# Kernel optimization log

Measured on AMD Instinct MI355X. Metric: run time of the kernel, lower is better.

The kernel has to match this reference:

```python
import jax, jax.numpy as jnp
import numpy as np

N = 1 << 20          # rays (1024x1024 image)
H = 128              # SDF MLP hidden dim
NEAR, FAR = 0.2, 2.0
ALPHA = 100.0
ITERS = 32           # sphere_march iters
EPS = 0.005
TP_BATCH = 32        # throughput batch_size
RAND_U = 0.5         # fixed replacement for random.random() in throughput


def setup_inputs() -> dict:
    key = jax.random.key(0)
    ks = jax.random.split(key, 6)
    def w(k, shape):
        return jax.random.normal(k, shape, jnp.float32) * (1.0 / np.sqrt(shape[0]))
    return {
        "rays": jax.random.normal(ks[0], (N, 6), jnp.float32),
        # SDF MLP: 3 -> H -> H -> 1 (output squeezed to scalar per point)
        "W1": w(ks[1], (3, H)), "b1": jnp.zeros((H,), jnp.float32),
        "W2": w(ks[2], (H, H)), "b2": jnp.zeros((H,), jnp.float32),
        "W3": w(ks[3], (H, 1)), "b3": jnp.zeros((1,), jnp.float32),
        # reflectance MLP: concat(pts, dir)=6 -> H -> 3
        "R1": w(ks[4], (6, H)), "rb1": jnp.zeros((H,), jnp.float32),
        "R2": w(ks[5], (H, 3)), "rb2": jnp.zeros((3,), jnp.float32),
    }


def _sdf(x, W1, b1, W2, b2, W3, b3):
    h = jax.nn.relu(x @ W1 + b1)
    h = jax.nn.relu(h @ W2 + b2)
    return (h @ W3 + b3)[..., 0]          # [N]


def _refl(x, d, R1, rb1, R2, rb2):
    h = jax.nn.relu(jnp.concatenate([x, d], axis=-1) @ R1 + rb1)
    return h @ R2 + rb2                    # [N, 3]


def reference(rays, W1, b1, W2, b2, W3, b3, R1, rb1, R2, rb2):
    r_o, r_d = rays[..., :3], rays[..., 3:]
    sg = jax.lax.stop_gradient
    # marching loops run under torch.no_grad -> use stop_gradient'd operands
    ro_s, rd_s = sg(r_o), sg(r_d)
    sdf_ng = lambda p: _sdf(p, sg(W1), sg(b1), sg(W2), sg(b2), sg(W3), sg(b3))

    # ---- sphere_march ----
    def march_body(i, carry):
        hits, cd = carry                                  # [N,1] bool, [N,1] f32
        dist = sdf_ng(ro_s + rd_s * cd)[..., None]
        hits = hits | ((dist < EPS) & (cd >= NEAR) & (cd <= FAR))
        cd = jnp.where(hits, cd, cd + dist)
        return hits, cd

    hits0 = jnp.zeros((rays.shape[0], 1), bool)
    cd0 = jnp.full((rays.shape[0], 1), NEAR, jnp.float32)
    hits, cd = jax.lax.fori_loop(0, ITERS, march_body, (hits0, cd0))

    pts = r_o + r_d * cd                                  # grads flow via r_o, r_d
    rgb = _refl(pts, r_d, R1, rb1, R2, rb2)               # [N,3]
    out = jnp.where(hits, rgb, jnp.zeros_like(rgb))

    # ---- throughput ----
    max_t = FAR + RAND_U * (2.0 / TP_BATCH)
    step = max_t / TP_BATCH

    def tp_body(i, carry):
        curr_min, idxs = carry                            # [N] f32, [N] i32
        sd = sdf_ng(ro_s + (step * (i + 1)) * rd_s)
        idxs = jnp.where(sd < curr_min, i + 1, idxs)
        curr_min = jnp.minimum(curr_min, sd)
        return curr_min, idxs

    sd0 = sdf_ng(ro_s)
    _, idxs = jax.lax.fori_loop(0, TP_BATCH, tp_body,
                                (sd0, jnp.zeros(sd0.shape, jnp.int32)))
    best_pos = r_o + idxs[..., None].astype(jnp.float32) * step * r_d
    tput = _sdf(best_pos, W1, b1, W2, b2, W3, b3)         # [N]

    return jnp.concatenate([out, -ALPHA * tput[..., None]], axis=-1)  # [N,4]
```

## Files before the change

### kernel.cpp

```cpp
#include <hip/hip_runtime.h>

typedef __attribute__((ext_vector_type(8))) short bf16x8;
typedef __attribute__((ext_vector_type(4))) float f32x4;
typedef __attribute__((ext_vector_type(2))) float f32x2;

constexpr int   HD      = 128;
constexpr float T_NEAR  = 0.2f;
constexpr float T_FAR   = 2.0f;
constexpr float ALPHA_C = 100.0f;
constexpr int   MARCH_N = 32;
constexpr float HIT_EPS = 0.005f;
constexpr int   TP_N    = 32;
constexpr float STEP    = 0.0634765625f;

__device__ __forceinline__ unsigned short f2bf(float x) {
  unsigned u = __float_as_uint(x);
  unsigned r = 0x7fffu + ((u >> 16) & 1u);
  return (unsigned short)((u + r) >> 16);
}

union U8 { bf16x8 v; uint4 u4; unsigned short us[8]; };

__device__ __forceinline__ f32x2 pk_fma(f32x2 a, f32x2 b, f32x2 c) {
  f32x2 d;
  asm("v_pk_fma_f32 %0, %1, %2, %3" : "=v"(d) : "v"(a), "v"(b), "v"(c));
  return d;
}

__device__ __forceinline__ unsigned pack_relu_pair(f32x2 h) {
  unsigned u0 = __float_as_uint(h.x) + 0x8000u;
  unsigned u1 = __float_as_uint(h.y) + 0x8000u;
  unsigned w, r;
  asm("v_perm_b32 %0, %1, %2, %3" : "=v"(w) : "v"(u1), "v"(u0), "s"(0x07060302u));
  asm("v_pk_max_i16 %0, %1, %2" : "=v"(r) : "v"(w), "v"(0u));
  return r;
}

__global__ void pack_w2(const float* __restrict__ W2,
                        unsigned short* __restrict__ hi,
                        unsigned short* __restrict__ lo) {
  int idx = blockIdx.x * 256 + threadIdx.x;
  int j = idx & 7, l = (idx >> 3) & 63, t = (idx >> 9) & 7, s = idx >> 12;
  int m = 16 * t + (l & 15);
  int k = 32 * s + (l >> 4) * 8 + j;
  float w = W2[k * HD + m];
  unsigned short h = f2bf(w);
  float hf = __uint_as_float(((unsigned)h) << 16);
  hi[idx] = h;
  lo[idx] = f2bf(w - hf);
}

__device__ __forceinline__ float sdf_fast(float t,
    const bf16x8 (&w2f)[4][8], const f32x2 (&ap)[16], const f32x2 (&cp)[16],
    const f32x4 (&b2f)[8], const f32x2 (&w3p)[16], float b3v)
{
  f32x2 t2; t2.x = t; t2.y = t;
  U8 B[4];
  #pragma unroll
  for (int s = 0; s < 4; ++s) {
    unsigned w0 = pack_relu_pair(pk_fma(cp[4*s+0], t2, ap[4*s+0]));
    unsigned w1 = pack_relu_pair(pk_fma(cp[4*s+1], t2, ap[4*s+1]));
    unsigned w2 = pack_relu_pair(pk_fma(cp[4*s+2], t2, ap[4*s+2]));
    unsigned w3 = pack_relu_pair(pk_fma(cp[4*s+3], t2, ap[4*s+3]));
    uint4 u; u.x = w0; u.y = w1; u.z = w2; u.w = w3;
    B[s].u4 = u;
  }

  f32x4 acc[8];
  #pragma unroll
  for (int u = 0; u < 8; ++u)
    acc[u] = __builtin_amdgcn_mfma_f32_16x16x32_bf16(w2f[0][u], B[0].v, b2f[u], 0, 0, 0);
  #pragma unroll
  for (int s = 1; s < 4; ++s)
    #pragma unroll
    for (int u = 0; u < 8; ++u)
      acc[u] = __builtin_amdgcn_mfma_f32_16x16x32_bf16(w2f[s][u], B[s].v, acc[u], 0, 0, 0);

  f32x2 e0; e0.x = 0.f; e0.y = 0.f;
  f32x2 e1 = e0, e2 = e0, e3 = e0;
  #pragma unroll
  for (int u = 0; u < 8; ++u) {
    f32x4 y = acc[u];
    f32x2 lo; lo.x = fmaxf(y.x, 0.f); lo.y = fmaxf(y.y, 0.f);
    f32x2 hi; hi.x = fmaxf(y.z, 0.f); hi.y = fmaxf(y.w, 0.f);
    if (u & 1) { e2 = pk_fma(lo, w3p[2*u], e2); e3 = pk_fma(hi, w3p[2*u+1], e3); }
    else       { e0 = pk_fma(lo, w3p[2*u], e0); e1 = pk_fma(hi, w3p[2*u+1], e1); }
  }
  float d = (e0.x + e0.y) + (e1.x + e1.y) + ((e2.x + e2.y) + (e3.x + e3.y));
  d += __shfl_xor(d, 16);
  d += __shfl_xor(d, 32);
  return d + b3v;
}

__device__ float sdf_precise(float t, int lane,
    const bf16x8 (&w2f)[4][8], const f32x2 (&ap)[16], const f32x2 (&cp)[16],
    const f32x4 (&b2f)[8], const f32x2 (&w3p)[16], float b3v,
    const unsigned short* __restrict__ wlo)
{
  U8 HH[4], HL[4];
  #pragma unroll
  for (int s = 0; s < 4; ++s) {
    #pragma unroll
    for (int p = 0; p < 4; ++p) {
      float h0 = fmaxf(fmaf(cp[4*s+p].x, t, ap[4*s+p].x), 0.f);
      float h1 = fmaxf(fmaf(cp[4*s+p].y, t, ap[4*s+p].y), 0.f);
      unsigned short hb0 = f2bf(h0), hb1 = f2bf(h1);
      float r0 = h0 - __uint_as_float(((unsigned)hb0) << 16);
      float r1 = h1 - __uint_as_float(((unsigned)hb1) << 16);
      HH[s].us[2*p]     = hb0;      HH[s].us[2*p + 1] = hb1;
      HL[s].us[2*p]     = f2bf(r0); HL[s].us[2*p + 1] = f2bf(r1);
    }
  }

  const bf16x8* wloF = (const bf16x8*)wlo;
  f32x4 acc[8];
  #pragma unroll
  for (int u = 0; u < 8; ++u)
    acc[u] = __builtin_amdgcn_mfma_f32_16x16x32_bf16(w2f[0][u], HH[0].v, b2f[u], 0, 0, 0);
  #pragma unroll
  for (int s = 0; s < 4; ++s) {
    #pragma unroll
    for (int u = 0; u < 8; ++u) {
      bf16x8 wl = wloF[(s * 8 + u) * 64 + lane];
      if (s > 0)
        acc[u] = __builtin_amdgcn_mfma_f32_16x16x32_bf16(w2f[s][u], HH[s].v, acc[u], 0, 0, 0);
      acc[u] = __builtin_amdgcn_mfma_f32_16x16x32_bf16(wl, HH[s].v, acc[u], 0, 0, 0);
      acc[u] = __builtin_amdgcn_mfma_f32_16x16x32_bf16(w2f[s][u], HL[s].v, acc[u], 0, 0, 0);
    }
  }

  f32x2 e0; e0.x = 0.f; e0.y = 0.f;
  f32x2 e1 = e0, e2 = e0, e3 = e0;
  #pragma unroll
  for (int u = 0; u < 8; ++u) {
    f32x4 y = acc[u];
    f32x2 lo; lo.x = fmaxf(y.x, 0.f); lo.y = fmaxf(y.y, 0.f);
    f32x2 hi; hi.x = fmaxf(y.z, 0.f); hi.y = fmaxf(y.w, 0.f);
    if (u & 1) { e2 = pk_fma(lo, w3p[2*u], e2); e3 = pk_fma(hi, w3p[2*u+1], e3); }
    else       { e0 = pk_fma(lo, w3p[2*u], e0); e1 = pk_fma(hi, w3p[2*u+1], e1); }
  }
  float d = (e0.x + e0.y) + (e1.x + e1.y) + ((e2.x + e2.y) + (e3.x + e3.y));
  d += __shfl_xor(d, 16);
  d += __shfl_xor(d, 32);
  return d + b3v;
}

__global__ __launch_bounds__(256, 1)
void render(const float* __restrict__ rays,
            const float* __restrict__ W1, const float* __restrict__ b1,
            const float* __restrict__ b2, const float* __restrict__ W3,
            const float* __restrict__ b3,
            const float* __restrict__ R1, const float* __restrict__ rb1,
            const float* __restrict__ R2, const float* __restrict__ rb2,
            const unsigned short* __restrict__ whi,
            const unsigned short* __restrict__ wlo,
            float* __restrict__ out, int nrays)
{
  const int tid  = threadIdx.x;
  const int lane = tid & 63;
  const int q    = lane >> 4;
  const int wv   = tid >> 6;
  const int ray  = blockIdx.x * 64 + wv * 16 + (lane & 15);

  bf16x8 w2f[4][8];
  const bf16x8* whiF = (const bf16x8*)whi;
  #pragma unroll
  for (int s = 0; s < 4; ++s)
    #pragma unroll
    for (int u = 0; u < 8; ++u)
      w2f[s][u] = whiF[(s * 8 + u) * 64 + lane];

  const float rox = rays[ray * 6 + 0];
  const float roy = rays[ray * 6 + 1];
  const float roz = rays[ray * 6 + 2];
  const float rdx = rays[ray * 6 + 3];
  const float rdy = rays[ray * 6 + 4];
  const float rdz = rays[ray * 6 + 5];
  const float b3v = b3[0];

  f32x2 ap[16], cp[16];
  #pragma unroll
  for (int s = 0; s < 4; ++s)
    #pragma unroll
    for (int p = 0; p < 4; ++p) {
      int k0 = 32 * s + 8 * q + 2 * p;
      int k1 = k0 + 1;
      float x0 = W1[k0], y0 = W1[HD + k0], z0 = W1[2 * HD + k0];
      float x1 = W1[k1], y1 = W1[HD + k1], z1 = W1[2 * HD + k1];
      f32x2 a, c;
      a.x = fmaf(x0, rox, fmaf(y0, roy, fmaf(z0, roz, b1[k0])));
      a.y = fmaf(x1, rox, fmaf(y1, roy, fmaf(z1, roz, b1[k1])));
      c.x = fmaf(x0, rdx, fmaf(y0, rdy, z0 * rdz));
      c.y = fmaf(x1, rdx, fmaf(y1, rdy, z1 * rdz));
      ap[4 * s + p] = a;
      cp[4 * s + p] = c;
    }

  f32x4 b2f[8];
  f32x2 w3p[16];
  #pragma unroll
  for (int u = 0; u < 8; ++u) {
    int n0 = 16 * u + 4 * q;
    f32x4 bb; bb.x = b2[n0]; bb.y = b2[n0 + 1]; bb.z = b2[n0 + 2]; bb.w = b2[n0 + 3];
    b2f[u] = bb;
    f32x2 wa; wa.x = W3[n0];     wa.y = W3[n0 + 1];
    f32x2 wb; wb.x = W3[n0 + 2]; wb.y = W3[n0 + 3];
    w3p[2 * u] = wa; w3p[2 * u + 1] = wb;
  }

  float cd = T_NEAR;
  bool hit = false;
  #pragma unroll 1
  for (int it = 0; it < MARCH_N; ++it) {
    float d = sdf_fast(cd, w2f, ap, cp, b2f, w3p, b3v);
    bool nh = (d < HIT_EPS) && (cd >= T_NEAR) && (cd <= T_FAR);
    hit = hit || nh;
    cd = hit ? cd : cd + d;
    if (__ballot(!hit) == 0ull) break;
  }

  const float ptx = fmaf(rdx, cd, rox);
  const float pty = fmaf(rdy, cd, roy);
  const float ptz = fmaf(rdz, cd, roz);
  float cr = 0.f, cg = 0.f, cb = 0.f;
  {
    int jb = q * 32;
    #pragma unroll 1
    for (int jj = 0; jj < 32; ++jj) {
      int j = jb + jj;
      float h = fmaf(R1[0 * HD + j], ptx,
                fmaf(R1[1 * HD + j], pty,
                fmaf(R1[2 * HD + j], ptz,
                fmaf(R1[3 * HD + j], rdx,
                fmaf(R1[4 * HD + j], rdy,
                fmaf(R1[5 * HD + j], rdz, rb1[j]))))));
      h = fmaxf(h, 0.f);
      cr = fmaf(h, R2[j * 3 + 0], cr);
      cg = fmaf(h, R2[j * 3 + 1], cg);
      cb = fmaf(h, R2[j * 3 + 2], cb);
    }
    cr += __shfl_xor(cr, 16); cr += __shfl_xor(cr, 32);
    cg += __shfl_xor(cg, 16); cg += __shfl_xor(cg, 32);
    cb += __shfl_xor(cb, 16); cb += __shfl_xor(cb, 32);
    cr += rb2[0]; cg += rb2[1]; cb += rb2[2];
  }

  float mn = sdf_fast(0.f, w2f, ap, cp, b2f, w3p, b3v);
  int idx = 0;
  float ts = 0.f;
  #pragma unroll 1
  for (int s = 1; s <= TP_N; ++s) {
    ts += STEP;
    float d = sdf_fast(ts, w2f, ap, cp, b2f, w3p, b3v);
    if (d < mn) { mn = d; idx = s; }
  }

  const float tb = STEP * (float)idx;
  const float tput = sdf_precise(tb, lane, w2f, ap, cp, b2f, w3p, b3v, wlo);

  if (q == 0) {
    float4 o;
    o.x = hit ? cr : 0.f;
    o.y = hit ? cg : 0.f;
    o.z = hit ? cb : 0.f;
    o.w = -ALPHA_C * tput;
    ((float4*)out)[ray] = o;
  }
}

extern "C" void kernel_launch(void* const* d_in, const int* in_sizes, int n_in,
                              void* d_out, int out_size, void* d_ws, size_t ws_size,
                              hipStream_t stream) {
  const float* rays = (const float*)d_in[0];
  const float* W1  = (const float*)d_in[1];
  const float* b1  = (const float*)d_in[2];
  const float* W2  = (const float*)d_in[3];
  const float* b2  = (const float*)d_in[4];
  const float* W3  = (const float*)d_in[5];
  const float* b3  = (const float*)d_in[6];
  const float* R1  = (const float*)d_in[7];
  const float* rb1 = (const float*)d_in[8];
  const float* R2  = (const float*)d_in[9];
  const float* rb2 = (const float*)d_in[10];

  unsigned short* whi = (unsigned short*)d_ws;
  unsigned short* wlo = whi + 128 * 128;

  const int nrays = in_sizes[0] / 6;

  hipLaunchKernelGGL(pack_w2, dim3(64), dim3(256), 0, stream, W2, whi, wlo);
  hipLaunchKernelGGL(render, dim3(nrays / 64), dim3(256), 0, stream,
                     rays, W1, b1, b2, W3, b3, R1, rb1, R2, rb2,
                     whi, wlo, (float*)d_out, nrays);
}
```

Before: 3.413 ms.

## Process two ray groups per wave with interleaved MFMA chains

```diff
diff --git a/kernel.cpp b/kernel.cpp
--- a/kernel.cpp
+++ b/kernel.cpp
@@ -50,32 +50,8 @@
   lo[idx] = f2bf(w - hf);
 }
 
-__device__ __forceinline__ float sdf_fast(float t,
-    const bf16x8 (&w2f)[4][8], const f32x2 (&ap)[16], const f32x2 (&cp)[16],
-    const f32x4 (&b2f)[8], const f32x2 (&w3p)[16], float b3v)
-{
-  f32x2 t2; t2.x = t; t2.y = t;
-  U8 B[4];
-  #pragma unroll
-  for (int s = 0; s < 4; ++s) {
-    unsigned w0 = pack_relu_pair(pk_fma(cp[4*s+0], t2, ap[4*s+0]));
-    unsigned w1 = pack_relu_pair(pk_fma(cp[4*s+1], t2, ap[4*s+1]));
-    unsigned w2 = pack_relu_pair(pk_fma(cp[4*s+2], t2, ap[4*s+2]));
-    unsigned w3 = pack_relu_pair(pk_fma(cp[4*s+3], t2, ap[4*s+3]));
-    uint4 u; u.x = w0; u.y = w1; u.z = w2; u.w = w3;
-    B[s].u4 = u;
-  }
-
-  f32x4 acc[8];
-  #pragma unroll
-  for (int u = 0; u < 8; ++u)
-    acc[u] = __builtin_amdgcn_mfma_f32_16x16x32_bf16(w2f[0][u], B[0].v, b2f[u], 0, 0, 0);
-  #pragma unroll
-  for (int s = 1; s < 4; ++s)
-    #pragma unroll
-    for (int u = 0; u < 8; ++u)
-      acc[u] = __builtin_amdgcn_mfma_f32_16x16x32_bf16(w2f[s][u], B[s].v, acc[u], 0, 0, 0);
-
+__device__ __forceinline__ float sdf_reduce(const f32x4 (&acc)[8],
+                                            const f32x2 (&w3p)[16], float b3v) {
   f32x2 e0; e0.x = 0.f; e0.y = 0.f;
   f32x2 e1 = e0, e2 = e0, e3 = e0;
   #pragma unroll
@@ -92,7 +68,51 @@
   return d + b3v;
 }
 
-__device__ float sdf_precise(float t, int lane,
+__device__ __forceinline__ void sdf_fast_dual(float tA, float tB,
+    const bf16x8 (&w2f)[4][8],
+    const f32x2 (&apA)[16], const f32x2 (&cpA)[16],
+    const f32x2 (&apB)[16], const f32x2 (&cpB)[16],
+    const f32x4 (&b2f)[8], const f32x2 (&w3p)[16], float b3v,
+    float& dA, float& dB)
+{
+  f32x2 tA2; tA2.x = tA; tA2.y = tA;
+  f32x2 tB2; tB2.x = tB; tB2.y = tB;
+  U8 BA[4], BB[4];
+  #pragma unroll
+  for (int s = 0; s < 4; ++s) {
+    uint4 ua;
+    ua.x = pack_relu_pair(pk_fma(cpA[4*s+0], tA2, apA[4*s+0]));
+    ua.y = pack_relu_pair(pk_fma(cpA[4*s+1], tA2, apA[4*s+1]));
+    ua.z = pack_relu_pair(pk_fma(cpA[4*s+2], tA2, apA[4*s+2]));
+    ua.w = pack_relu_pair(pk_fma(cpA[4*s+3], tA2, apA[4*s+3]));
+    BA[s].u4 = ua;
+    uint4 ub;
+    ub.x = pack_relu_pair(pk_fma(cpB[4*s+0], tB2, apB[4*s+0]));
+    ub.y = pack_relu_pair(pk_fma(cpB[4*s+1], tB2, apB[4*s+1]));
+    ub.z = pack_relu_pair(pk_fma(cpB[4*s+2], tB2, apB[4*s+2]));
+    ub.w = pack_relu_pair(pk_fma(cpB[4*s+3], tB2, apB[4*s+3]));
+    BB[s].u4 = ub;
+  }
+
+  f32x4 accA[8], accB[8];
+  #pragma unroll
+  for (int u = 0; u < 8; ++u) {
+    accA[u] = __builtin_amdgcn_mfma_f32_16x16x32_bf16(w2f[0][u], BA[0].v, b2f[u], 0, 0, 0);
+    accB[u] = __builtin_amdgcn_mfma_f32_16x16x32_bf16(w2f[0][u], BB[0].v, b2f[u], 0, 0, 0);
+  }
+  #pragma unroll
+  for (int s = 1; s < 4; ++s)
+    #pragma unroll
+    for (int u = 0; u < 8; ++u) {
+      accA[u] = __builtin_amdgcn_mfma_f32_16x16x32_bf16(w2f[s][u], BA[s].v, accA[u], 0, 0, 0);
+      accB[u] = __builtin_amdgcn_mfma_f32_16x16x32_bf16(w2f[s][u], BB[s].v, accB[u], 0, 0, 0);
+    }
+
+  dA = sdf_reduce(accA, w3p, b3v);
+  dB = sdf_reduce(accB, w3p, b3v);
+}
+
+__device__ __forceinline__ float sdf_precise(float t, int lane,
     const bf16x8 (&w2f)[4][8], const f32x2 (&ap)[16], const f32x2 (&cp)[16],
     const f32x4 (&b2f)[8], const f32x2 (&w3p)[16], float b3v,
     const unsigned short* __restrict__ wlo)
@@ -129,20 +149,7 @@
     }
   }
 
-  f32x2 e0; e0.x = 0.f; e0.y = 0.f;
-  f32x2 e1 = e0, e2 = e0, e3 = e0;
-  #pragma unroll
-  for (int u = 0; u < 8; ++u) {
-    f32x4 y = acc[u];
-    f32x2 lo; lo.x = fmaxf(y.x, 0.f); lo.y = fmaxf(y.y, 0.f);
-    f32x2 hi; hi.x = fmaxf(y.z, 0.f); hi.y = fmaxf(y.w, 0.f);
-    if (u & 1) { e2 = pk_fma(lo, w3p[2*u], e2); e3 = pk_fma(hi, w3p[2*u+1], e3); }
-    else       { e0 = pk_fma(lo, w3p[2*u], e0); e1 = pk_fma(hi, w3p[2*u+1], e1); }
-  }
-  float d = (e0.x + e0.y) + (e1.x + e1.y) + ((e2.x + e2.y) + (e3.x + e3.y));
-  d += __shfl_xor(d, 16);
-  d += __shfl_xor(d, 32);
-  return d + b3v;
+  return sdf_reduce(acc, w3p, b3v);
 }
 
 __global__ __launch_bounds__(256, 1)
@@ -160,7 +167,8 @@
   const int lane = tid & 63;
   const int q    = lane >> 4;
   const int wv   = tid >> 6;
-  const int ray  = blockIdx.x * 64 + wv * 16 + (lane & 15);
+  const int rayA = blockIdx.x * 128 + wv * 32 + (lane & 15);
+  const int rayB = rayA + 16;
 
   bf16x8 w2f[4][8];
   const bf16x8* whiF = (const bf16x8*)whi;
@@ -170,30 +178,42 @@
     for (int u = 0; u < 8; ++u)
       w2f[s][u] = whiF[(s * 8 + u) * 64 + lane];
 
-  const float rox = rays[ray * 6 + 0];
-  const float roy = rays[ray * 6 + 1];
-  const float roz = rays[ray * 6 + 2];
-  const float rdx = rays[ray * 6 + 3];
-  const float rdy = rays[ray * 6 + 4];
-  const float rdz = rays[ray * 6 + 5];
+  const float roxA = rays[rayA * 6 + 0];
+  const float royA = rays[rayA * 6 + 1];
+  const float rozA = rays[rayA * 6 + 2];
+  const float rdxA = rays[rayA * 6 + 3];
+  const float rdyA = rays[rayA * 6 + 4];
+  const float rdzA = rays[rayA * 6 + 5];
+  const float roxB = rays[rayB * 6 + 0];
+  const float royB = rays[rayB * 6 + 1];
+  const float rozB = rays[rayB * 6 + 2];
+  const float rdxB = rays[rayB * 6 + 3];
+  const float rdyB = rays[rayB * 6 + 4];
+  const float rdzB = rays[rayB * 6 + 5];
   const float b3v = b3[0];
 
-  f32x2 ap[16], cp[16];
+  f32x2 apA[16], cpA[16], apB[16], cpB[16];
   #pragma unroll
   for (int s = 0; s < 4; ++s)
     #pragma unroll
     for (int p = 0; p < 4; ++p) {
       int k0 = 32 * s + 8 * q + 2 * p;
       int k1 = k0 + 1;
-      float x0 = W1[k0], y0 = W1[HD + k0], z0 = W1[2 * HD + k0];
-      float x1 = W1[k1], y1 = W1[HD + k1], z1 = W1[2 * HD + k1];
+      float x0 = W1[k0], y0 = W1[HD + k0], z0 = W1[2 * HD + k0], g0 = b1[k0];
+      float x1 = W1[k1], y1 = W1[HD + k1], z1 = W1[2 * HD + k1], g1 = b1[k1];
       f32x2 a, c;
-      a.x = fmaf(x0, rox, fmaf(y0, roy, fmaf(z0, roz, b1[k0])));
-      a.y = fmaf(x1, rox, fmaf(y1, roy, fmaf(z1, roz, b1[k1])));
-      c.x = fmaf(x0, rdx, fmaf(y0, rdy, z0 * rdz));
-      c.y = fmaf(x1, rdx, fmaf(y1, rdy, z1 * rdz));
-      ap[4 * s + p] = a;
-      cp[4 * s + p] = c;
+      a.x = fmaf(x0, roxA, fmaf(y0, royA, fmaf(z0, rozA, g0)));
+      a.y = fmaf(x1, roxA, fmaf(y1, royA, fmaf(z1, rozA, g1)));
+      c.x = fmaf(x0, rdxA, fmaf(y0, rdyA, z0 * rdzA));
+      c.y = fmaf(x1, rdxA, fmaf(y1, rdyA, z1 * rdzA));
+      apA[4 * s + p] = a;
+      cpA[4 * s + p] = c;
+      a.x = fmaf(x0, roxB, fmaf(y0, royB, fmaf(z0, rozB, g0)));
+      a.y = fmaf(x1, roxB, fmaf(y1, royB, fmaf(z1, rozB, g1)));
+      c.x = fmaf(x0, rdxB, fmaf(y0, rdyB, z0 * rdzB));
+      c.y = fmaf(x1, rdxB, fmaf(y1, rdyB, z1 * rdzB));
+      apB[4 * s + p] = a;
+      cpB[4 * s + p] = c;
     }
 
   f32x4 b2f[8];
@@ -208,63 +228,89 @@
     w3p[2 * u] = wa; w3p[2 * u + 1] = wb;
   }
 
-  float cd = T_NEAR;
-  bool hit = false;
+  float cdA = T_NEAR, cdB = T_NEAR;
+  bool hitA = false, hitB = false;
   #pragma unroll 1
   for (int it = 0; it < MARCH_N; ++it) {
-    float d = sdf_fast(cd, w2f, ap, cp, b2f, w3p, b3v);
-    bool nh = (d < HIT_EPS) && (cd >= T_NEAR) && (cd <= T_FAR);
-    hit = hit || nh;
-    cd = hit ? cd : cd + d;
-    if (__ballot(!hit) == 0ull) break;
-  }
-
-  const float ptx = fmaf(rdx, cd, rox);
-  const float pty = fmaf(rdy, cd, roy);
-  const float ptz = fmaf(rdz, cd, roz);
-  float cr = 0.f, cg = 0.f, cb = 0.f;
+    float dA, dB;
+    sdf_fast_dual(cdA, cdB, w2f, apA, cpA, apB, cpB, b2f, w3p, b3v, dA, dB);
+    bool nhA = (dA < HIT_EPS) && (cdA >= T_NEAR) && (cdA <= T_FAR);
+    hitA = hitA || nhA;
+    cdA = hitA ? cdA : cdA + dA;
+    bool nhB = (dB < HIT_EPS) && (cdB >= T_NEAR) && (cdB <= T_FAR);
+    hitB = hitB || nhB;
+    cdB = hitB ? cdB : cdB + dB;
+    if ((__ballot(!hitA) | __ballot(!hitB)) == 0ull) break;
+  }
+
+  const float ptxA = fmaf(rdxA, cdA, roxA);
+  const float ptyA = fmaf(rdyA, cdA, royA);
+  const float ptzA = fmaf(rdzA, cdA, rozA);
+  const float ptxB = fmaf(rdxB, cdB, roxB);
+  const float ptyB = fmaf(rdyB, cdB, royB);
+  const float ptzB = fmaf(rdzB, cdB, rozB);
+  float crA = 0.f, cgA = 0.f, cbA = 0.f;
+  float crB = 0.f, cgB = 0.f, cbB = 0.f;
   {
     int jb = q * 32;
     #pragma unroll 1
     for (int jj = 0; jj < 32; ++jj) {
       int j = jb + jj;
-      float h = fmaf(R1[0 * HD + j], ptx,
-                fmaf(R1[1 * HD + j], pty,
-                fmaf(R1[2 * HD + j], ptz,
-                fmaf(R1[3 * HD + j], rdx,
-                fmaf(R1[4 * HD + j], rdy,
-                fmaf(R1[5 * HD + j], rdz, rb1[j]))))));
-      h = fmaxf(h, 0.f);
-      cr = fmaf(h, R2[j * 3 + 0], cr);
-      cg = fmaf(h, R2[j * 3 + 1], cg);
-      cb = fmaf(h, R2[j * 3 + 2], cb);
-    }
-    cr += __shfl_xor(cr, 16); cr += __shfl_xor(cr, 32);
-    cg += __shfl_xor(cg, 16); cg += __shfl_xor(cg, 32);
-    cb += __shfl_xor(cb, 16); cb += __shfl_xor(cb, 32);
-    cr += rb2[0]; cg += rb2[1]; cb += rb2[2];
-  }
-
-  float mn = sdf_fast(0.f, w2f, ap, cp, b2f, w3p, b3v);
-  int idx = 0;
+      float r0 = R1[0 * HD + j], r1 = R1[1 * HD + j], r2 = R1[2 * HD + j];
+      float r3 = R1[3 * HD + j], r4 = R1[4 * HD + j], r5 = R1[5 * HD + j];
+      float rb = rb1[j];
+      float hA = fmaf(r0, ptxA, fmaf(r1, ptyA, fmaf(r2, ptzA,
+                 fmaf(r3, rdxA, fmaf(r4, rdyA, fmaf(r5, rdzA, rb))))));
+      hA = fmaxf(hA, 0.f);
+      float hB = fmaf(r0, ptxB, fmaf(r1, ptyB, fmaf(r2, ptzB,
+                 fmaf(r3, rdxB, fmaf(r4, rdyB, fmaf(r5, rdzB, rb))))));
+      hB = fmaxf(hB, 0.f);
+      float s0 = R2[j * 3 + 0], s1 = R2[j * 3 + 1], s2 = R2[j * 3 + 2];
+      crA = fmaf(hA, s0, crA); cgA = fmaf(hA, s1, cgA); cbA = fmaf(hA, s2, cbA);
+      crB = fmaf(hB, s0, crB); cgB = fmaf(hB, s1, cgB); cbB = fmaf(hB, s2, cbB);
+    }
+    crA += __shfl_xor(crA, 16); crA += __shfl_xor(crA, 32);
+    cgA += __shfl_xor(cgA, 16); cgA += __shfl_xor(cgA, 32);
+    cbA += __shfl_xor(cbA, 16); cbA += __shfl_xor(cbA, 32);
+    crB += __shfl_xor(crB, 16); crB += __shfl_xor(crB, 32);
+    cgB += __shfl_xor(cgB, 16); cgB += __shfl_xor(cgB, 32);
+    cbB += __shfl_xor(cbB, 16); cbB += __shfl_xor(cbB, 32);
+    crA += rb2[0]; cgA += rb2[1]; cbA += rb2[2];
+    crB += rb2[0]; cgB += rb2[1]; cbB += rb2[2];
+  }
+
+  float mnA, mnB;
+  sdf_fast_dual(0.f, 0.f, w2f, apA, cpA, apB, cpB, b2f, w3p, b3v, mnA, mnB);
+  int idxA = 0, idxB = 0;
   float ts = 0.f;
   #pragma unroll 1
   for (int s = 1; s <= TP_N; ++s) {
     ts += STEP;
-    float d = sdf_fast(ts, w2f, ap, cp, b2f, w3p, b3v);
-    if (d < mn) { mn = d; idx = s; }
-  }
-
-  const float tb = STEP * (float)idx;
-  const float tput = sdf_precise(tb, lane, w2f, ap, cp, b2f, w3p, b3v, wlo);
+    float dA, dB;
+    sdf_fast_dual(ts, ts, w2f, apA, cpA, apB, cpB, b2f, w3p, b3v, dA, dB);
+    if (dA < mnA) { mnA = dA; idxA = s; }
+    if (dB < mnB) { mnB = dB; idxB = s; }
+  }
+
+  const float tbA = STEP * (float)idxA;
+  const float tputA = sdf_precise(tbA, lane, w2f, apA, cpA, b2f, w3p, b3v, wlo);
+  const float tbB = STEP * (float)idxB;
+  const float tputB = sdf_precise(tbB, lane, w2f, apB, cpB, b2f, w3p, b3v, wlo);
 
   if (q == 0) {
     float4 o;
-    o.x = hit ? cr : 0.f;
-    o.y = hit ? cg : 0.f;
-    o.z = hit ? cb : 0.f;
-    o.w = -ALPHA_C * tput;
-    ((float4*)out)[ray] = o;
+    o.x = hitA ? crA : 0.f;
+    o.y = hitA ? cgA : 0.f;
+    o.z = hitA ? cbA : 0.f;
+    o.w = -ALPHA_C * tputA;
+    ((float4*)out)[rayA] = o;
+  } else if (q == 1) {
+    float4 o;
+    o.x = hitB ? crB : 0.f;
+    o.y = hitB ? cgB : 0.f;
+    o.z = hitB ? cbB : 0.f;
+    o.w = -ALPHA_C * tputB;
+    ((float4*)out)[rayB] = o;
   }
 }
 
@@ -289,7 +335,7 @@
   const int nrays = in_sizes[0] / 6;
 
   hipLaunchKernelGGL(pack_w2, dim3(64), dim3(256), 0, stream, W2, whi, wlo);
-  hipLaunchKernelGGL(render, dim3(nrays / 64), dim3(256), 0, stream,
+  hipLaunchKernelGGL(render, dim3(nrays / 128), dim3(256), 0, stream,
                      rays, W1, b1, b2, W3, b3, R1, rb1, R2, rb2,
                      whi, wlo, (float*)d_out, nrays);
 }
```

Measured after the change: 3.465 ms. Within noise of the previous version (+1.5%).

## Move b2/W3 to LDS and interleave packing to allow two blocks per CU

Applied to the files above, without the earlier changes.

```diff
diff --git a/kernel.cpp b/kernel.cpp
--- a/kernel.cpp
+++ b/kernel.cpp
@@ -50,41 +50,20 @@
   lo[idx] = f2bf(w - hf);
 }
 
-__device__ __forceinline__ float sdf_fast(float t,
-    const bf16x8 (&w2f)[4][8], const f32x2 (&ap)[16], const f32x2 (&cp)[16],
-    const f32x4 (&b2f)[8], const f32x2 (&w3p)[16], float b3v)
-{
-  f32x2 t2; t2.x = t; t2.y = t;
-  U8 B[4];
-  #pragma unroll
-  for (int s = 0; s < 4; ++s) {
-    unsigned w0 = pack_relu_pair(pk_fma(cp[4*s+0], t2, ap[4*s+0]));
-    unsigned w1 = pack_relu_pair(pk_fma(cp[4*s+1], t2, ap[4*s+1]));
-    unsigned w2 = pack_relu_pair(pk_fma(cp[4*s+2], t2, ap[4*s+2]));
-    unsigned w3 = pack_relu_pair(pk_fma(cp[4*s+3], t2, ap[4*s+3]));
-    uint4 u; u.x = w0; u.y = w1; u.z = w2; u.w = w3;
-    B[s].u4 = u;
-  }
-
-  f32x4 acc[8];
-  #pragma unroll
-  for (int u = 0; u < 8; ++u)
-    acc[u] = __builtin_amdgcn_mfma_f32_16x16x32_bf16(w2f[0][u], B[0].v, b2f[u], 0, 0, 0);
-  #pragma unroll
-  for (int s = 1; s < 4; ++s)
-    #pragma unroll
-    for (int u = 0; u < 8; ++u)
-      acc[u] = __builtin_amdgcn_mfma_f32_16x16x32_bf16(w2f[s][u], B[s].v, acc[u], 0, 0, 0);
-
+__device__ __forceinline__ float sdf_reduce(const f32x4 (&acc)[8],
+                                            const float* lw, int q, float b3v) {
   f32x2 e0; e0.x = 0.f; e0.y = 0.f;
   f32x2 e1 = e0, e2 = e0, e3 = e0;
   #pragma unroll
   for (int u = 0; u < 8; ++u) {
+    f32x4 w = *(const f32x4*)(lw + 128 + 16 * u + 4 * q);
+    f32x2 wa; wa.x = w.x; wa.y = w.y;
+    f32x2 wb; wb.x = w.z; wb.y = w.w;
     f32x4 y = acc[u];
     f32x2 lo; lo.x = fmaxf(y.x, 0.f); lo.y = fmaxf(y.y, 0.f);
     f32x2 hi; hi.x = fmaxf(y.z, 0.f); hi.y = fmaxf(y.w, 0.f);
-    if (u & 1) { e2 = pk_fma(lo, w3p[2*u], e2); e3 = pk_fma(hi, w3p[2*u+1], e3); }
-    else       { e0 = pk_fma(lo, w3p[2*u], e0); e1 = pk_fma(hi, w3p[2*u+1], e1); }
+    if (u & 1) { e2 = pk_fma(lo, wa, e2); e3 = pk_fma(hi, wb, e3); }
+    else       { e0 = pk_fma(lo, wa, e0); e1 = pk_fma(hi, wb, e1); }
   }
   float d = (e0.x + e0.y) + (e1.x + e1.y) + ((e2.x + e2.y) + (e3.x + e3.y));
   d += __shfl_xor(d, 16);
@@ -92,14 +71,52 @@
   return d + b3v;
 }
 
-__device__ float sdf_precise(float t, int lane,
+__device__ __forceinline__ float sdf_fast(float t,
     const bf16x8 (&w2f)[4][8], const f32x2 (&ap)[16], const f32x2 (&cp)[16],
-    const f32x4 (&b2f)[8], const f32x2 (&w3p)[16], float b3v,
+    const float* lw, int q, float b3v)
+{
+  f32x2 t2; t2.x = t; t2.y = t;
+  f32x4 acc[8];
+  {
+    U8 B;
+    uint4 u4;
+    u4.x = pack_relu_pair(pk_fma(cp[0], t2, ap[0]));
+    u4.y = pack_relu_pair(pk_fma(cp[1], t2, ap[1]));
+    u4.z = pack_relu_pair(pk_fma(cp[2], t2, ap[2]));
+    u4.w = pack_relu_pair(pk_fma(cp[3], t2, ap[3]));
+    B.u4 = u4;
+    #pragma unroll
+    for (int u = 0; u < 8; ++u) {
+      f32x4 c = *(const f32x4*)(lw + 16 * u + 4 * q);
+      acc[u] = __builtin_amdgcn_mfma_f32_16x16x32_bf16(w2f[0][u], B.v, c, 0, 0, 0);
+    }
+  }
+  #pragma unroll
+  for (int s = 1; s < 4; ++s) {
+    U8 B;
+    uint4 u4;
+    u4.x = pack_relu_pair(pk_fma(cp[4*s+0], t2, ap[4*s+0]));
+    u4.y = pack_relu_pair(pk_fma(cp[4*s+1], t2, ap[4*s+1]));
+    u4.z = pack_relu_pair(pk_fma(cp[4*s+2], t2, ap[4*s+2]));
+    u4.w = pack_relu_pair(pk_fma(cp[4*s+3], t2, ap[4*s+3]));
+    B.u4 = u4;
+    #pragma unroll
+    for (int u = 0; u < 8; ++u)
+      acc[u] = __builtin_amdgcn_mfma_f32_16x16x32_bf16(w2f[s][u], B.v, acc[u], 0, 0, 0);
+  }
+  return sdf_reduce(acc, lw, q, b3v);
+}
+
+__device__ __forceinline__ float sdf_precise(float t, int lane,
+    const bf16x8 (&w2f)[4][8], const f32x2 (&ap)[16], const f32x2 (&cp)[16],
+    const float* lw, int q, float b3v,
     const unsigned short* __restrict__ wlo)
 {
-  U8 HH[4], HL[4];
+  const bf16x8* wloF = (const bf16x8*)wlo;
+  f32x4 acc[8];
   #pragma unroll
   for (int s = 0; s < 4; ++s) {
+    U8 HH, HL;
     #pragma unroll
     for (int p = 0; p < 4; ++p) {
       float h0 = fmaxf(fmaf(cp[4*s+p].x, t, ap[4*s+p].x), 0.f);
@@ -107,45 +124,29 @@
       unsigned short hb0 = f2bf(h0), hb1 = f2bf(h1);
       float r0 = h0 - __uint_as_float(((unsigned)hb0) << 16);
       float r1 = h1 - __uint_as_float(((unsigned)hb1) << 16);
-      HH[s].us[2*p]     = hb0;      HH[s].us[2*p + 1] = hb1;
-      HL[s].us[2*p]     = f2bf(r0); HL[s].us[2*p + 1] = f2bf(r1);
-    }
-  }
-
-  const bf16x8* wloF = (const bf16x8*)wlo;
-  f32x4 acc[8];
-  #pragma unroll
-  for (int u = 0; u < 8; ++u)
-    acc[u] = __builtin_amdgcn_mfma_f32_16x16x32_bf16(w2f[0][u], HH[0].v, b2f[u], 0, 0, 0);
-  #pragma unroll
-  for (int s = 0; s < 4; ++s) {
+      HH.us[2*p]     = hb0;      HH.us[2*p + 1] = hb1;
+      HL.us[2*p]     = f2bf(r0); HL.us[2*p + 1] = f2bf(r1);
+    }
+    if (s == 0) {
+      #pragma unroll
+      for (int u = 0; u < 8; ++u) {
+        f32x4 c = *(const f32x4*)(lw + 16 * u + 4 * q);
+        acc[u] = __builtin_amdgcn_mfma_f32_16x16x32_bf16(w2f[0][u], HH.v, c, 0, 0, 0);
+      }
+    }
     #pragma unroll
     for (int u = 0; u < 8; ++u) {
       bf16x8 wl = wloF[(s * 8 + u) * 64 + lane];
       if (s > 0)
-        acc[u] = __builtin_amdgcn_mfma_f32_16x16x32_bf16(w2f[s][u], HH[s].v, acc[u], 0, 0, 0);
-      acc[u] = __builtin_amdgcn_mfma_f32_16x16x32_bf16(wl, HH[s].v, acc[u], 0, 0, 0);
-      acc[u] = __builtin_amdgcn_mfma_f32_16x16x32_bf16(w2f[s][u], HL[s].v, acc[u], 0, 0, 0);
-    }
-  }
-
-  f32x2 e0; e0.x = 0.f; e0.y = 0.f;
-  f32x2 e1 = e0, e2 = e0, e3 = e0;
-  #pragma unroll
-  for (int u = 0; u < 8; ++u) {
-    f32x4 y = acc[u];
-    f32x2 lo; lo.x = fmaxf(y.x, 0.f); lo.y = fmaxf(y.y, 0.f);
-    f32x2 hi; hi.x = fmaxf(y.z, 0.f); hi.y = fmaxf(y.w, 0.f);
-    if (u & 1) { e2 = pk_fma(lo, w3p[2*u], e2); e3 = pk_fma(hi, w3p[2*u+1], e3); }
-    else       { e0 = pk_fma(lo, w3p[2*u], e0); e1 = pk_fma(hi, w3p[2*u+1], e1); }
-  }
-  float d = (e0.x + e0.y) + (e1.x + e1.y) + ((e2.x + e2.y) + (e3.x + e3.y));
-  d += __shfl_xor(d, 16);
-  d += __shfl_xor(d, 32);
-  return d + b3v;
-}
-
-__global__ __launch_bounds__(256, 1)
+        acc[u] = __builtin_amdgcn_mfma_f32_16x16x32_bf16(w2f[s][u], HH.v, acc[u], 0, 0, 0);
+      acc[u] = __builtin_amdgcn_mfma_f32_16x16x32_bf16(wl, HH.v, acc[u], 0, 0, 0);
+      acc[u] = __builtin_amdgcn_mfma_f32_16x16x32_bf16(w2f[s][u], HL.v, acc[u], 0, 0, 0);
+    }
+  }
+  return sdf_reduce(acc, lw, q, b3v);
+}
+
+__global__ __launch_bounds__(256, 2)
 void render(const float* __restrict__ rays,
             const float* __restrict__ W1, const float* __restrict__ b1,
             const float* __restrict__ b2, const float* __restrict__ W3,
@@ -156,11 +157,17 @@
             const unsigned short* __restrict__ wlo,
             float* __restrict__ out, int nrays)
 {
+  __shared__ __align__(16) float lwb[4][256];
+
   const int tid  = threadIdx.x;
   const int lane = tid & 63;
   const int q    = lane >> 4;
   const int wv   = tid >> 6;
   const int ray  = blockIdx.x * 64 + wv * 16 + (lane & 15);
+
+  float* lw = &lwb[wv][0];
+  if (lane < 32) ((float4*)lw)[lane] = ((const float4*)b2)[lane];
+  else           ((float4*)lw)[lane] = ((const float4*)W3)[lane - 32];
 
   bf16x8 w2f[4][8];
   const bf16x8* whiF = (const bf16x8*)whi;
@@ -196,23 +203,11 @@
       cp[4 * s + p] = c;
     }
 
-  f32x4 b2f[8];
-  f32x2 w3p[16];
-  #pragma unroll
-  for (int u = 0; u < 8; ++u) {
-    int n0 = 16 * u + 4 * q;
-    f32x4 bb; bb.x = b2[n0]; bb.y = b2[n0 + 1]; bb.z = b2[n0 + 2]; bb.w = b2[n0 + 3];
-    b2f[u] = bb;
-    f32x2 wa; wa.x = W3[n0];     wa.y = W3[n0 + 1];
-    f32x2 wb; wb.x = W3[n0 + 2]; wb.y = W3[n0 + 3];
-    w3p[2 * u] = wa; w3p[2 * u + 1] = wb;
-  }
-
   float cd = T_NEAR;
   bool hit = false;
   #pragma unroll 1
   for (int it = 0; it < MARCH_N; ++it) {
-    float d = sdf_fast(cd, w2f, ap, cp, b2f, w3p, b3v);
+    float d = sdf_fast(cd, w2f, ap, cp, lw, q, b3v);
     bool nh = (d < HIT_EPS) && (cd >= T_NEAR) && (cd <= T_FAR);
     hit = hit || nh;
     cd = hit ? cd : cd + d;
@@ -245,18 +240,18 @@
     cr += rb2[0]; cg += rb2[1]; cb += rb2[2];
   }
 
-  float mn = sdf_fast(0.f, w2f, ap, cp, b2f, w3p, b3v);
+  float mn = sdf_fast(0.f, w2f, ap, cp, lw, q, b3v);
   int idx = 0;
   float ts = 0.f;
   #pragma unroll 1
   for (int s = 1; s <= TP_N; ++s) {
     ts += STEP;
-    float d = sdf_fast(ts, w2f, ap, cp, b2f, w3p, b3v);
+    float d = sdf_fast(ts, w2f, ap, cp, lw, q, b3v);
     if (d < mn) { mn = d; idx = s; }
   }
 
   const float tb = STEP * (float)idx;
-  const float tput = sdf_precise(tb, lane, w2f, ap, cp, b2f, w3p, b3v, wlo);
+  const float tput = sdf_precise(tb, lane, w2f, ap, cp, lw, q, b3v, wlo);
 
   if (q == 0) {
     float4 o;
```

Result: slower. 5.268 ms (+54.4%).
